# Kernel optimization log

Measured on AMD Instinct MI355X. Metric: run time of the kernel, lower is better.

The kernel has to match this reference:

```python
import jax, jax.numpy as jnp
import numpy as np

D_MODEL = 512
HEAD = 64

def setup_inputs() -> dict:
    key = jax.random.key(0)
    ks = jax.random.split(key, 7)
    s_in = 1.0 / np.sqrt(D_MODEL)
    x = jax.random.normal(ks[0], (4, 4096, D_MODEL), dtype=jnp.float32)
    Wk = jax.random.uniform(ks[1], (D_MODEL, HEAD), jnp.float32, -s_in, s_in)
    bk = jax.random.uniform(ks[2], (HEAD,), jnp.float32, -s_in, s_in)
    Wq = jax.random.uniform(ks[3], (D_MODEL, HEAD), jnp.float32, -s_in, s_in)
    bq = jax.random.uniform(ks[4], (HEAD,), jnp.float32, -s_in, s_in)
    Wv = jax.random.uniform(ks[5], (D_MODEL, HEAD), jnp.float32, -s_in, s_in)
    bv = jax.random.uniform(ks[6], (HEAD,), jnp.float32, -s_in, s_in)
    return {"x": x, "Wk": Wk, "bk": bk, "Wq": Wq, "bq": bq, "Wv": Wv, "bv": bv}

def reference(x, Wk, bk, Wq, bq, Wv, bv):
    B, T, C = x.shape
    k = x @ Wk + bk            # [B,T,H]
    q = x @ Wq + bq            # [B,T,H]
    v = x @ Wv + bv            # [B,T,H]
    scale = C ** (-0.5)
    # NOTE: original computes k @ q^T (keys index rows), softmax over query axis
    w = jnp.einsum('bkh,bqh->bkq', k, q) * scale  # [B,T,T]
    w = jax.nn.softmax(w, axis=-1)
    out = jnp.einsum('bkq,bqh->bkh', w, v)        # [B,T,H]
    return out
```

## Files before the change

### kernel.cpp

```cpp
#include <hip/hip_runtime.h>


#define DM 512
#define HD 64
#define TSEQ 4096
#define KSCALE (1.4426950408889634f * 0.04419417382415922f)

typedef __attribute__((ext_vector_type(8))) __bf16 bf16x8;
typedef __attribute__((ext_vector_type(4))) __bf16 bf16x4;
typedef __attribute__((ext_vector_type(2))) __bf16 bf16x2;
typedef __attribute__((ext_vector_type(4))) float f32x4;
typedef __attribute__((ext_vector_type(16))) float f32x16;
typedef __attribute__((ext_vector_type(4))) unsigned int uint4v;

__device__ __forceinline__ float fast_exp2(float x) {
#if __has_builtin(__builtin_amdgcn_exp2f)
    return __builtin_amdgcn_exp2f(x);
#else
    return exp2f(x);
#endif
}

__device__ __forceinline__ bf16x8 ld_bf16x8(const unsigned short* p) {
    return __builtin_bit_cast(bf16x8, *(const uint4v*)p);
}
__device__ __forceinline__ f32x4 mfma16(bf16x8 a, bf16x8 b, f32x4 c) {
    return __builtin_amdgcn_mfma_f32_16x16x32_bf16(a, b, c, 0, 0, 0);
}
__device__ __forceinline__ f32x16 mfma32(bf16x8 a, bf16x8 b, f32x16 c) {
    return __builtin_amdgcn_mfma_f32_32x32x16_bf16(a, b, c, 0, 0, 0);
}

typedef const __attribute__((address_space(1))) unsigned int* gas_t;
typedef __attribute__((address_space(3))) unsigned int* las_t;
__device__ __forceinline__ void async_cp16(const void* g, void* l) {
    __builtin_amdgcn_global_load_lds((gas_t)(unsigned long long)g,
                                     (las_t)(unsigned int)(unsigned long long)l,
                                     16, 0, 0);
}

__global__ __launch_bounds__(256) void prep_wt(const float* __restrict__ Wk,
                                               const float* __restrict__ Wq,
                                               const float* __restrict__ Wv,
                                               unsigned short* __restrict__ WT) {
    int e = blockIdx.x * 256 + threadIdx.x;
    int m = e >> 15;
    int idx = e & 32767;
    int h = idx >> 9;
    int cc = idx & 511;
    const float* W = (m == 0) ? Wk : ((m == 1) ? Wq : Wv);
    float v = W[cc * HD + h];
    if (m == 0) v *= KSCALE;
    ((__bf16*)WT)[m * 32768 + h * DM + cc] = (__bf16)v;
}

__global__ __launch_bounds__(512, 4) void proj(const float* __restrict__ x,
                                               const unsigned short* __restrict__ WT,
                                               const float* __restrict__ bk,
                                               const float* __restrict__ bq,
                                               const float* __restrict__ bv,
                                               unsigned short* __restrict__ Kw,
                                               unsigned short* __restrict__ Qw,
                                               unsigned short* __restrict__ VTw) {
    __shared__ alignas(16) float xs[16384];
    const int tid = threadIdx.x;
    const int wv = tid >> 6, lane = tid & 63;
    const int c = lane & 15, quad = lane >> 4;
    const int ng = wv & 3, rg = wv >> 2;
    const int bx = blockIdx.x;
    const int n0 = ng * 16;

#pragma unroll
    for (int r = 0; r < 8; ++r) {
        int cid = r * 512 + tid;
        int row = cid >> 7, pos = cid & 127;
        int g = (pos & ~7) | ((pos ^ row) & 7);
        async_cp16((const char*)x + (size_t)(bx * 32 + row) * 2048 + g * 16,
                   (char*)xs + r * 8192 + wv * 1024);
    }
    __builtin_amdgcn_s_waitcnt(0x0f70);
    __syncthreads();

    const int arow = rg * 16 + c;
    const unsigned short* wtb = WT + (n0 + c) * DM + quad * 8;
    f32x4 acc[3];
#pragma unroll
    for (int m = 0; m < 3; ++m) acc[m] = (f32x4){0.f, 0.f, 0.f, 0.f};

#pragma unroll
    for (int ks = 0; ks < 16; ++ks) {
        int p0 = ks * 8 + quad * 2;
        int sp0 = (p0 & ~7) | ((p0 ^ arow) & 7);
        int sp1 = ((p0 + 1) & ~7) | (((p0 + 1) ^ arow) & 7);
        f32x4 xa = *(const f32x4*)((const char*)xs + arow * 2048 + sp0 * 16);
        f32x4 xb = *(const f32x4*)((const char*)xs + arow * 2048 + sp1 * 16);
        bf16x8 af;
        af[0] = (__bf16)xa[0]; af[1] = (__bf16)xa[1]; af[2] = (__bf16)xa[2]; af[3] = (__bf16)xa[3];
        af[4] = (__bf16)xb[0]; af[5] = (__bf16)xb[1]; af[6] = (__bf16)xb[2]; af[7] = (__bf16)xb[3];
#pragma unroll
        for (int m = 0; m < 3; ++m) {
            bf16x8 bf = ld_bf16x8(wtb + m * 32768 + ks * 32);
            acc[m] = mfma16(af, bf, acc[m]);
        }
    }

    const int row0 = bx * 32 + rg * 16 + quad * 4;
#pragma unroll
    for (int m = 0; m < 3; ++m) {
        const float* bp = (m == 0) ? bk : ((m == 1) ? bq : bv);
        float bias = bp[n0 + c];
        if (m == 0) bias *= KSCALE;
        if (m < 2) {
            __bf16* dst = (__bf16*)((m == 0) ? Kw : Qw);
#pragma unroll
            for (int r = 0; r < 4; ++r)
                dst[(row0 + r) * HD + n0 + c] = (__bf16)(acc[m][r] + bias);
        } else {
            bf16x4 pk;
#pragma unroll
            for (int r = 0; r < 4; ++r) pk[r] = (__bf16)(acc[m][r] + bias);
            int b = bx >> 7;
            int rowb = (bx & 127) * 32 + rg * 16 + quad * 4;
            *(bf16x4*)(VTw + ((size_t)(b * 64 + n0 + c)) * TSEQ + rowb) = pk;
        }
    }
}

__global__ __launch_bounds__(512, 2) void attn(const unsigned short* __restrict__ Kw,
                                               const unsigned short* __restrict__ Qw,
                                               const unsigned short* __restrict__ VTw,
                                               float* __restrict__ Op,
                                               float* __restrict__ Lp) {
    __shared__ alignas(16) char smem[65536];

    const int tid = threadIdx.x;
    const int wv = tid >> 6, lane = tid & 63;
    const int l5 = lane >> 5, l31 = lane & 31;
    const int rg = wv >> 2, jc = wv & 3;
    const int bx = blockIdx.x;
    const int batch = bx >> 6, js = (bx >> 5) & 1, tile = bx & 31;
    const int rowbase = batch * TSEQ + tile * 128;

    bf16x8 kf[2][4];
#pragma unroll
    for (int it = 0; it < 2; ++it) {
        const unsigned short* kp = Kw + (size_t)(rowbase + rg * 64 + it * 32 + l31) * HD;
#pragma unroll
        for (int ks = 0; ks < 4; ++ks) kf[it][ks] = ld_bf16x8(kp + ks * 16 + l5 * 8);
    }

    const int jrow = jc * 32 + l31;
    int qoff[4];
#pragma unroll
    for (int ks = 0; ks < 4; ++ks)
        qoff[ks] = jrow * 128 + (((ks * 2 + l5) ^ (jrow & 7)) * 16);
    int voff[2][2];
#pragma unroll
    for (int ht = 0; ht < 2; ++ht)
#pragma unroll
        for (int k2 = 0; k2 < 2; ++k2) {
            int h = ht * 32 + l31;
            voff[ht][k2] = h * 256 + (((jc * 4 + k2 * 2 + l5) ^ (h & 15)) * 16);
        }

    const char* qg = (const char*)(Qw + (size_t)(batch * TSEQ + js * 2048) * HD);
    const char* vg = (const char*)(VTw + (size_t)batch * 64 * TSEQ + js * 2048);
    const int L1 = 512 + tid;
    const int qgo0 = ((tid >> 3) * 128) + (((tid & 7) ^ ((tid >> 3) & 7)) * 16);
    const int qgo1 = ((L1 >> 3) * 128) + (((L1 & 7) ^ ((L1 >> 3) & 7)) * 16);
    const int vgo0 = ((tid >> 4) * 8192) + (((tid & 15) ^ ((tid >> 4) & 15)) * 16);
    const int vgo1 = ((L1 >> 4) * 8192) + (((L1 & 15) ^ ((L1 >> 4) & 15)) * 16);

    f32x16 o00, o01, o10, o11;
#pragma unroll
    for (int r = 0; r < 16; ++r) { o00[r] = 0.f; o01[r] = 0.f; o10[r] = 0.f; o11[r] = 0.f; }
    float lac0 = 0.f, lac1 = 0.f;

    {
        char* nb = smem;
        async_cp16(qg + qgo0, nb + wv * 1024);
        async_cp16(qg + qgo1, nb + 8192 + wv * 1024);
        async_cp16(vg + vgo0, nb + 16384 + wv * 1024);
        async_cp16(vg + vgo1, nb + 16384 + 8192 + wv * 1024);
    }

    for (int jt = 0; jt < 16; ++jt) {
        __builtin_amdgcn_s_waitcnt(0x0f70);
        __syncthreads();
        const char* cb = smem + (jt & 1) * 32768;
        if (jt < 15) {
            char* nb = smem + ((jt + 1) & 1) * 32768;
            async_cp16(qg + (jt + 1) * 16384 + qgo0, nb + wv * 1024);
            async_cp16(qg + (jt + 1) * 16384 + qgo1, nb + 8192 + wv * 1024);
            async_cp16(vg + (jt + 1) * 256 + vgo0, nb + 16384 + wv * 1024);
            async_cp16(vg + (jt + 1) * 256 + vgo1, nb + 16384 + 8192 + wv * 1024);
            __builtin_amdgcn_sched_barrier(0);
        }
        const unsigned short* QL = (const unsigned short*)cb;
        const unsigned short* VL = (const unsigned short*)(cb + 16384);

        f32x16 s0, s1;
#pragma unroll
        for (int r = 0; r < 16; ++r) { s0[r] = 0.f; s1[r] = 0.f; }
#pragma unroll
        for (int ks = 0; ks < 4; ++ks) {
            bf16x8 qa = ld_bf16x8((const unsigned short*)((const char*)QL + qoff[ks]));
            s0 = mfma32(qa, kf[0][ks], s0);
            s1 = mfma32(qa, kf[1][ks], s1);
        }

        unsigned int pk0[8], pk1[8];
#pragma unroll
        for (int m = 0; m < 8; ++m) {
            float a0 = fast_exp2(s0[2 * m]), a1 = fast_exp2(s0[2 * m + 1]);
            float b0 = fast_exp2(s1[2 * m]), b1 = fast_exp2(s1[2 * m + 1]);
            lac0 += a0 + a1;
            lac1 += b0 + b1;
            bf16x2 ta; ta[0] = (__bf16)a0; ta[1] = (__bf16)a1;
            bf16x2 tb; tb[0] = (__bf16)b0; tb[1] = (__bf16)b1;
            pk0[m] = __builtin_bit_cast(unsigned int, ta);
            pk1[m] = __builtin_bit_cast(unsigned int, tb);
        }

#pragma unroll
        for (int k2 = 0; k2 < 2; ++k2) {
            bf16x8 pb0, pb1;
            {
                unsigned int A0 = pk0[k2 * 4 + 0], A1 = pk0[k2 * 4 + 1];
                unsigned int B0 = pk0[k2 * 4 + 2], B1 = pk0[k2 * 4 + 3];
                unsigned int t0 = l5 ? A0 : B0, t1 = l5 ? A1 : B1;
                unsigned int r0 = (unsigned int)__shfl_xor((int)t0, 32, 64);
                unsigned int r1 = (unsigned int)__shfl_xor((int)t1, 32, 64);
                uint4v u;
                u[0] = l5 ? r0 : A0; u[1] = l5 ? r1 : A1;
                u[2] = l5 ? B0 : r0; u[3] = l5 ? B1 : r1;
                pb0 = __builtin_bit_cast(bf16x8, u);
            }
            {
                unsigned int A0 = pk1[k2 * 4 + 0], A1 = pk1[k2 * 4 + 1];
                unsigned int B0 = pk1[k2 * 4 + 2], B1 = pk1[k2 * 4 + 3];
                unsigned int t0 = l5 ? A0 : B0, t1 = l5 ? A1 : B1;
                unsigned int r0 = (unsigned int)__shfl_xor((int)t0, 32, 64);
                unsigned int r1 = (unsigned int)__shfl_xor((int)t1, 32, 64);
                uint4v u;
                u[0] = l5 ? r0 : A0; u[1] = l5 ? r1 : A1;
                u[2] = l5 ? B0 : r0; u[3] = l5 ? B1 : r1;
                pb1 = __builtin_bit_cast(bf16x8, u);
            }
            bf16x8 vf0 = ld_bf16x8((const unsigned short*)((const char*)VL + voff[0][k2]));
            bf16x8 vf1 = ld_bf16x8((const unsigned short*)((const char*)VL + voff[1][k2]));
            o00 = mfma32(vf0, pb0, o00);
            o01 = mfma32(vf0, pb1, o01);
            o10 = mfma32(vf1, pb0, o10);
            o11 = mfma32(vf1, pb1, o11);
        }
    }

    lac0 += __shfl_xor(lac0, 32, 64);
    lac1 += __shfl_xor(lac1, 32, 64);
    __syncthreads();
    float* OCp = (float*)smem;
    float* ldsl = (float*)(smem + 34816);
    if (l5 == 0) {
        ldsl[jc * 128 + rg * 64 + l31] = lac0;
        ldsl[jc * 128 + rg * 64 + 32 + l31] = lac1;
    }

#pragma unroll
    for (int ph = 0; ph < 4; ++ph) {
        const int ht = ph >> 1, ih = ph & 1;
        __syncthreads();
        if (rg == ih) {
            const f32x16 oa = ht ? o10 : o00;
            const f32x16 ob = ht ? o11 : o01;
#pragma unroll
            for (int r = 0; r < 16; ++r) {
                int hr = (r & 3) + 8 * (r >> 2) + 4 * l5;
                OCp[(jc * 32 + hr) * 68 + l31] = oa[r];
                OCp[(jc * 32 + hr) * 68 + 32 + l31] = ob[r];
            }
        }
        __syncthreads();
#pragma unroll
        for (int rep = 0; rep < 4; ++rep) {
            int idx = rep * 512 + tid;
            int i = idx >> 5, hr = idx & 31;
            float v = OCp[(0 * 32 + hr) * 68 + i] + OCp[(1 * 32 + hr) * 68 + i]
                    + OCp[(2 * 32 + hr) * 68 + i] + OCp[(3 * 32 + hr) * 68 + i];
            Op[(size_t)js * 1048576 + (size_t)(rowbase + ih * 64 + i) * HD + ht * 32 + hr] = v;
        }
        if (ph == 0 && tid < 128) {
            float L = ldsl[tid] + ldsl[128 + tid] + ldsl[256 + tid] + ldsl[384 + tid];
            Lp[js * 16384 + rowbase + tid] = L;
        }
    }
}

__global__ __launch_bounds__(512) void fin(const float* __restrict__ Op,
                                           const float* __restrict__ Lp,
                                           float* __restrict__ out) {
    int idx = blockIdx.x * 512 + threadIdx.x;
    int e = idx * 4;
    int row = e >> 6;
    f32x4 a = *(const f32x4*)(Op + e);
    f32x4 b = *(const f32x4*)(Op + 1048576 + e);
    float L = Lp[row] + Lp[16384 + row];
    f32x4 r;
#pragma unroll
    for (int k = 0; k < 4; ++k) r[k] = (a[k] + b[k]) / L;
    *(f32x4*)(out + e) = r;
}

extern "C" void kernel_launch(void* const* d_in, const int* in_sizes, int n_in,
                              void* d_out, int out_size, void* d_ws, size_t ws_size,
                              hipStream_t stream) {
    (void)in_sizes; (void)n_in; (void)out_size; (void)ws_size;
    const float* x  = (const float*)d_in[0];
    const float* Wk = (const float*)d_in[1];
    const float* bk = (const float*)d_in[2];
    const float* Wq = (const float*)d_in[3];
    const float* bq = (const float*)d_in[4];
    const float* Wv = (const float*)d_in[5];
    const float* bv = (const float*)d_in[6];

    char* ws = (char*)d_ws;
    unsigned short* WT  = (unsigned short*)(ws);
    unsigned short* Kw  = (unsigned short*)(ws + 196608);
    unsigned short* Qw  = (unsigned short*)(ws + 2293760);
    unsigned short* VTw = (unsigned short*)(ws + 4390912);
    float* Opart        = (float*)(ws + 6488064);
    float* Lpart        = (float*)(ws + 14876672);
    float* outp = (float*)d_out;

    hipLaunchKernelGGL(prep_wt, dim3(384), dim3(256), 0, stream, Wk, Wq, Wv, WT);
    hipLaunchKernelGGL(proj, dim3(512), dim3(512), 0, stream,
                       x, WT, bk, bq, bv, Kw, Qw, VTw);
    hipLaunchKernelGGL(attn, dim3(256), dim3(512), 0, stream, Kw, Qw, VTw, Opart, Lpart);
    hipLaunchKernelGGL(fin, dim3(512), dim3(512), 0, stream, Opart, Lpart, outp);
}
```

Baseline: 136.7 us.

## Drop split-KV and finalize kernel; stream Q/V directly from global into registers

The attention kernel no longer splits the query axis across two blocks with a separate combine kernel. Each block now owns 64 key rows and loops over all 4096 queries, with each of the 8 waves handling its own 32-query slice. Q and V fragments are loaded straight from global memory into registers with a double-buffered prefetch, replacing the LDS async-copy pipeline and its per-step barriers. The 8-way partial reduction, normalisation and output store happen in-kernel, and a block index remap spreads batches across XCDs. The cost is more redundant global traffic per block, since each wave reads uncoalesced Q/V rows without LDS sharing, and latency is no longer hidden by LDS staging.

```diff
diff --git a/kernel.cpp b/kernel.cpp
--- a/kernel.cpp
+++ b/kernel.cpp
@@ -129,84 +129,63 @@
 __global__ __launch_bounds__(512, 2) void attn(const unsigned short* __restrict__ Kw,
                                                const unsigned short* __restrict__ Qw,
                                                const unsigned short* __restrict__ VTw,
-                                               float* __restrict__ Op,
-                                               float* __restrict__ Lp) {
-    __shared__ alignas(16) char smem[65536];
+                                               float* __restrict__ out) {
+    __shared__ float OCp[8 * 32 * 34];
+    __shared__ float ldsl[512];
+    __shared__ float Lrec[64];
 
     const int tid = threadIdx.x;
     const int wv = tid >> 6, lane = tid & 63;
     const int l5 = lane >> 5, l31 = lane & 31;
-    const int rg = wv >> 2, jc = wv & 3;
+    const int jc = wv;
     const int bx = blockIdx.x;
-    const int batch = bx >> 6, js = (bx >> 5) & 1, tile = bx & 31;
-    const int rowbase = batch * TSEQ + tile * 128;
-
-    bf16x8 kf[2][4];
-#pragma unroll
-    for (int it = 0; it < 2; ++it) {
-        const unsigned short* kp = Kw + (size_t)(rowbase + rg * 64 + it * 32 + l31) * HD;
-#pragma unroll
-        for (int ks = 0; ks < 4; ++ks) kf[it][ks] = ld_bf16x8(kp + ks * 16 + l5 * 8);
-    }
-
-    const int jrow = jc * 32 + l31;
-    int qoff[4];
-#pragma unroll
-    for (int ks = 0; ks < 4; ++ks)
-        qoff[ks] = jrow * 128 + (((ks * 2 + l5) ^ (jrow & 7)) * 16);
-    int voff[2][2];
-#pragma unroll
-    for (int ht = 0; ht < 2; ++ht)
-#pragma unroll
-        for (int k2 = 0; k2 < 2; ++k2) {
-            int h = ht * 32 + l31;
-            voff[ht][k2] = h * 256 + (((jc * 4 + k2 * 2 + l5) ^ (h & 15)) * 16);
-        }
-
-    const char* qg = (const char*)(Qw + (size_t)(batch * TSEQ + js * 2048) * HD);
-    const char* vg = (const char*)(VTw + (size_t)batch * 64 * TSEQ + js * 2048);
-    const int L1 = 512 + tid;
-    const int qgo0 = ((tid >> 3) * 128) + (((tid & 7) ^ ((tid >> 3) & 7)) * 16);
-    const int qgo1 = ((L1 >> 3) * 128) + (((L1 & 7) ^ ((L1 >> 3) & 7)) * 16);
-    const int vgo0 = ((tid >> 4) * 8192) + (((tid & 15) ^ ((tid >> 4) & 15)) * 16);
-    const int vgo1 = ((L1 >> 4) * 8192) + (((L1 & 15) ^ ((L1 >> 4) & 15)) * 16);
+    const int lb = (bx & 7) * 32 + (bx >> 3);
+    const int batch = lb >> 6, tile = lb & 63;
+    const int ibase = batch * TSEQ + tile * 64;
+
+    bf16x8 kf0[4], kf1[4];
+    {
+        const unsigned short* kp0 = Kw + (size_t)(ibase + l31) * HD + l5 * 8;
+        const unsigned short* kp1 = Kw + (size_t)(ibase + 32 + l31) * HD + l5 * 8;
+#pragma unroll
+        for (int ks = 0; ks < 4; ++ks) {
+            kf0[ks] = ld_bf16x8(kp0 + ks * 16);
+            kf1[ks] = ld_bf16x8(kp1 + ks * 16);
+        }
+    }
+
+    const unsigned short* qp = Qw + (size_t)(batch * TSEQ + jc * 32 + l31) * HD + l5 * 8;
+    const unsigned short* vp = VTw + (size_t)(batch * 64 + l31) * TSEQ + jc * 32 + l5 * 8;
 
     f32x16 o00, o01, o10, o11;
 #pragma unroll
     for (int r = 0; r < 16; ++r) { o00[r] = 0.f; o01[r] = 0.f; o10[r] = 0.f; o11[r] = 0.f; }
     float lac0 = 0.f, lac1 = 0.f;
 
-    {
-        char* nb = smem;
-        async_cp16(qg + qgo0, nb + wv * 1024);
-        async_cp16(qg + qgo1, nb + 8192 + wv * 1024);
-        async_cp16(vg + vgo0, nb + 16384 + wv * 1024);
-        async_cp16(vg + vgo1, nb + 16384 + 8192 + wv * 1024);
-    }
-
-    for (int jt = 0; jt < 16; ++jt) {
-        __builtin_amdgcn_s_waitcnt(0x0f70);
-        __syncthreads();
-        const char* cb = smem + (jt & 1) * 32768;
-        if (jt < 15) {
-            char* nb = smem + ((jt + 1) & 1) * 32768;
-            async_cp16(qg + (jt + 1) * 16384 + qgo0, nb + wv * 1024);
-            async_cp16(qg + (jt + 1) * 16384 + qgo1, nb + 8192 + wv * 1024);
-            async_cp16(vg + (jt + 1) * 256 + vgo0, nb + 16384 + wv * 1024);
-            async_cp16(vg + (jt + 1) * 256 + vgo1, nb + 16384 + 8192 + wv * 1024);
-            __builtin_amdgcn_sched_barrier(0);
-        }
-        const unsigned short* QL = (const unsigned short*)cb;
-        const unsigned short* VL = (const unsigned short*)(cb + 16384);
+    bf16x8 qA[4], qB[4];
+#pragma unroll
+    for (int ks = 0; ks < 4; ++ks) qA[ks] = ld_bf16x8(qp + ks * 16);
+
+    auto STEP = [&](const bf16x8 (&qc)[4], bf16x8 (&qn)[4], int jt) {
+        const unsigned short* vb = vp + jt * 256;
+        bf16x8 v00 = ld_bf16x8(vb);
+        bf16x8 v01 = ld_bf16x8(vb + 16);
+        bf16x8 v10 = ld_bf16x8(vb + 32 * TSEQ);
+        bf16x8 v11 = ld_bf16x8(vb + 32 * TSEQ + 16);
 
         f32x16 s0, s1;
 #pragma unroll
         for (int r = 0; r < 16; ++r) { s0[r] = 0.f; s1[r] = 0.f; }
 #pragma unroll
         for (int ks = 0; ks < 4; ++ks) {
-            bf16x8 qa = ld_bf16x8((const unsigned short*)((const char*)QL + qoff[ks]));
-            s0 = mfma32(qa, kf[0][ks], s0);
-            s1 = mfma32(qa, kf[1][ks], s1);
+            s0 = mfma32(qc[ks], kf0[ks], s0);
+            s1 = mfma32(qc[ks], kf1[ks], s1);
+        }
+
+        if (jt + 1 < 16) {
+            const unsigned short* qb = qp + (jt + 1) * 16384;
+#pragma unroll
+            for (int ks = 0; ks < 4; ++ks) qn[ks] = ld_bf16x8(qb + ks * 16);
         }
 
         unsigned int pk0[8], pk1[8];
@@ -247,68 +226,57 @@
                 u[2] = l5 ? B0 : r0; u[3] = l5 ? B1 : r1;
                 pb1 = __builtin_bit_cast(bf16x8, u);
             }
-            bf16x8 vf0 = ld_bf16x8((const unsigned short*)((const char*)VL + voff[0][k2]));
-            bf16x8 vf1 = ld_bf16x8((const unsigned short*)((const char*)VL + voff[1][k2]));
+            bf16x8 vf0 = k2 ? v01 : v00;
+            bf16x8 vf1 = k2 ? v11 : v10;
             o00 = mfma32(vf0, pb0, o00);
             o01 = mfma32(vf0, pb1, o01);
             o10 = mfma32(vf1, pb0, o10);
             o11 = mfma32(vf1, pb1, o11);
         }
+    };
+
+#pragma unroll 1
+    for (int jt = 0; jt < 16; jt += 2) {
+        STEP(qA, qB, jt);
+        STEP(qB, qA, jt + 1);
     }
 
     lac0 += __shfl_xor(lac0, 32, 64);
     lac1 += __shfl_xor(lac1, 32, 64);
+    if (l5 == 0) {
+        ldsl[jc * 64 + l31] = lac0;
+        ldsl[jc * 64 + 32 + l31] = lac1;
+    }
     __syncthreads();
-    float* OCp = (float*)smem;
-    float* ldsl = (float*)(smem + 34816);
-    if (l5 == 0) {
-        ldsl[jc * 128 + rg * 64 + l31] = lac0;
-        ldsl[jc * 128 + rg * 64 + 32 + l31] = lac1;
-    }
+    if (tid < 64) {
+        float L = 0.f;
+#pragma unroll
+        for (int j = 0; j < 8; ++j) L += ldsl[j * 64 + tid];
+        Lrec[tid] = 1.0f / L;
+    }
+    __syncthreads();
 
 #pragma unroll
     for (int ph = 0; ph < 4; ++ph) {
-        const int ht = ph >> 1, ih = ph & 1;
+        const int ht = ph >> 1, it = ph & 1;
+        const f32x16 ov = (ph == 0) ? o00 : (ph == 1) ? o01 : (ph == 2) ? o10 : o11;
+#pragma unroll
+        for (int r = 0; r < 16; ++r) {
+            int hr = (r & 3) + 8 * (r >> 2) + 4 * l5;
+            OCp[(jc * 32 + hr) * 34 + l31] = ov[r];
+        }
         __syncthreads();
-        if (rg == ih) {
-            const f32x16 oa = ht ? o10 : o00;
-            const f32x16 ob = ht ? o11 : o01;
-#pragma unroll
-            for (int r = 0; r < 16; ++r) {
-                int hr = (r & 3) + 8 * (r >> 2) + 4 * l5;
-                OCp[(jc * 32 + hr) * 68 + l31] = oa[r];
-                OCp[(jc * 32 + hr) * 68 + 32 + l31] = ob[r];
-            }
-        }
-        __syncthreads();
-#pragma unroll
-        for (int rep = 0; rep < 4; ++rep) {
+#pragma unroll
+        for (int rep = 0; rep < 2; ++rep) {
             int idx = rep * 512 + tid;
             int i = idx >> 5, hr = idx & 31;
-            float v = OCp[(0 * 32 + hr) * 68 + i] + OCp[(1 * 32 + hr) * 68 + i]
-                    + OCp[(2 * 32 + hr) * 68 + i] + OCp[(3 * 32 + hr) * 68 + i];
-            Op[(size_t)js * 1048576 + (size_t)(rowbase + ih * 64 + i) * HD + ht * 32 + hr] = v;
-        }
-        if (ph == 0 && tid < 128) {
-            float L = ldsl[tid] + ldsl[128 + tid] + ldsl[256 + tid] + ldsl[384 + tid];
-            Lp[js * 16384 + rowbase + tid] = L;
-        }
-    }
-}
-
-__global__ __launch_bounds__(512) void fin(const float* __restrict__ Op,
-                                           const float* __restrict__ Lp,
-                                           float* __restrict__ out) {
-    int idx = blockIdx.x * 512 + threadIdx.x;
-    int e = idx * 4;
-    int row = e >> 6;
-    f32x4 a = *(const f32x4*)(Op + e);
-    f32x4 b = *(const f32x4*)(Op + 1048576 + e);
-    float L = Lp[row] + Lp[16384 + row];
-    f32x4 r;
-#pragma unroll
-    for (int k = 0; k < 4; ++k) r[k] = (a[k] + b[k]) / L;
-    *(f32x4*)(out + e) = r;
+            float s = 0.f;
+#pragma unroll
+            for (int j = 0; j < 8; ++j) s += OCp[(j * 32 + hr) * 34 + i];
+            out[(size_t)(ibase + it * 32 + i) * HD + ht * 32 + hr] = s * Lrec[it * 32 + i];
+        }
+        if (ph < 3) __syncthreads();
+    }
 }
 
 extern "C" void kernel_launch(void* const* d_in, const int* in_sizes, int n_in,
@@ -328,13 +296,10 @@
     unsigned short* Kw  = (unsigned short*)(ws + 196608);
     unsigned short* Qw  = (unsigned short*)(ws + 2293760);
     unsigned short* VTw = (unsigned short*)(ws + 4390912);
-    float* Opart        = (float*)(ws + 6488064);
-    float* Lpart        = (float*)(ws + 14876672);
     float* outp = (float*)d_out;
 
     hipLaunchKernelGGL(prep_wt, dim3(384), dim3(256), 0, stream, Wk, Wq, Wv, WT);
     hipLaunchKernelGGL(proj, dim3(512), dim3(512), 0, stream,
                        x, WT, bk, bq, bv, Kw, Qw, VTw);
-    hipLaunchKernelGGL(attn, dim3(256), dim3(512), 0, stream, Kw, Qw, VTw, Opart, Lpart);
-    hipLaunchKernelGGL(fin, dim3(512), dim3(512), 0, stream, Opart, Lpart, outp);
-}
+    hipLaunchKernelGGL(attn, dim3(256), dim3(512), 0, stream, Kw, Qw, VTw, outp);
+}
```

Measured after the change: 141.4 us. +3.5%, slower.

## Fuse split-K combine into attention via last-block atomic counter

Applied to the files above, without the earlier changes.

Removes the separate finalize kernel. Each attention block bumps a per-tile atomic counter after writing its partial output and row sums, and the second block to finish for a tile sums the two partials and normalizes them into the output. The counters are zeroed in the weight-prep kernel. This saves one kernel launch and its global round trip, at the cost of threadfences, an atomic per block, and the tail work landing on whichever block finishes last.

```diff
diff --git a/kernel.cpp b/kernel.cpp
--- a/kernel.cpp
+++ b/kernel.cpp
@@ -42,7 +42,9 @@
 __global__ __launch_bounds__(256) void prep_wt(const float* __restrict__ Wk,
                                                const float* __restrict__ Wq,
                                                const float* __restrict__ Wv,
-                                               unsigned short* __restrict__ WT) {
+                                               unsigned short* __restrict__ WT,
+                                               int* __restrict__ cnt) {
+    if (blockIdx.x == 0 && threadIdx.x < 128) cnt[threadIdx.x] = 0;
     int e = blockIdx.x * 256 + threadIdx.x;
     int m = e >> 15;
     int idx = e & 32767;
@@ -130,8 +132,11 @@
                                                const unsigned short* __restrict__ Qw,
                                                const unsigned short* __restrict__ VTw,
                                                float* __restrict__ Op,
-                                               float* __restrict__ Lp) {
+                                               float* __restrict__ Lp,
+                                               float* __restrict__ out,
+                                               int* __restrict__ cnt) {
     __shared__ alignas(16) char smem[65536];
+    __shared__ int lastflag;
 
     const int tid = threadIdx.x;
     const int wv = tid >> 6, lane = tid & 63;
@@ -294,21 +299,29 @@
             Lp[js * 16384 + rowbase + tid] = L;
         }
     }
-}
-
-__global__ __launch_bounds__(512) void fin(const float* __restrict__ Op,
-                                           const float* __restrict__ Lp,
-                                           float* __restrict__ out) {
-    int idx = blockIdx.x * 512 + threadIdx.x;
-    int e = idx * 4;
-    int row = e >> 6;
-    f32x4 a = *(const f32x4*)(Op + e);
-    f32x4 b = *(const f32x4*)(Op + 1048576 + e);
-    float L = Lp[row] + Lp[16384 + row];
-    f32x4 r;
-#pragma unroll
-    for (int k = 0; k < 4; ++k) r[k] = (a[k] + b[k]) / L;
-    *(f32x4*)(out + e) = r;
+
+    __syncthreads();
+    if (tid == 0) {
+        __threadfence();
+        lastflag = atomicAdd(&cnt[batch * 32 + tile], 1);
+    }
+    __syncthreads();
+    if (lastflag) {
+        __threadfence();
+#pragma unroll
+        for (int rep = 0; rep < 4; ++rep) {
+            int idx = rep * 512 + tid;
+            int rloc = idx >> 4, h4 = (idx & 15) * 4;
+            size_t row = (size_t)rowbase + rloc;
+            f32x4 a = *(const f32x4*)(Op + row * HD + h4);
+            f32x4 b = *(const f32x4*)(Op + 1048576 + row * HD + h4);
+            float L = Lp[row] + Lp[16384 + row];
+            f32x4 r;
+#pragma unroll
+            for (int k = 0; k < 4; ++k) r[k] = (a[k] + b[k]) / L;
+            *(f32x4*)(out + row * HD + h4) = r;
+        }
+    }
 }
 
 extern "C" void kernel_launch(void* const* d_in, const int* in_sizes, int n_in,
@@ -318,8 +331,8 @@
     const float* x  = (const float*)d_in[0];
     const float* Wk = (const float*)d_in[1];
     const float* bk = (const float*)d_in[2];
+    const float* bq = (const float*)d_in[4];
     const float* Wq = (const float*)d_in[3];
-    const float* bq = (const float*)d_in[4];
     const float* Wv = (const float*)d_in[5];
     const float* bv = (const float*)d_in[6];
 
@@ -330,11 +343,12 @@
     unsigned short* VTw = (unsigned short*)(ws + 4390912);
     float* Opart        = (float*)(ws + 6488064);
     float* Lpart        = (float*)(ws + 14876672);
+    int* cnt            = (int*)(ws + 15007744);
     float* outp = (float*)d_out;
 
-    hipLaunchKernelGGL(prep_wt, dim3(384), dim3(256), 0, stream, Wk, Wq, Wv, WT);
+    hipLaunchKernelGGL(prep_wt, dim3(384), dim3(256), 0, stream, Wk, Wq, Wv, WT, cnt);
     hipLaunchKernelGGL(proj, dim3(512), dim3(512), 0, stream,
                        x, WT, bk, bq, bv, Kw, Qw, VTw);
-    hipLaunchKernelGGL(attn, dim3(256), dim3(512), 0, stream, Kw, Qw, VTw, Opart, Lpart);
-    hipLaunchKernelGGL(fin, dim3(512), dim3(512), 0, stream, Opart, Lpart, outp);
-}
+    hipLaunchKernelGGL(attn, dim3(256), dim3(512), 0, stream,
+                       Kw, Qw, VTw, Opart, Lpart, outp, cnt);
+}
```

Result: slower. 156.6 us (+14.6%).
